# Performance work log

Measured on AMD Instinct MI355X. Metric: run time of the kernel, lower is better.

Reference implementation:

```python
import jax, jax.numpy as jnp
import numpy as np

D_MODEL = 2048
N_HEADS = 16
KV_HEADS = 4
HEAD_DIM = D_MODEL // N_HEADS  # 128
GROUP = N_HEADS // KV_HEADS    # 4
B, T = 2, 2048
KV_WIDTH = KV_HEADS * HEAD_DIM


def _alibi_bias(n_heads: int, t: int) -> jnp.ndarray:
    # standard alibi slopes: geometric sequence 2^(-8i/n)
    slopes = 2.0 ** (-8.0 * (np.arange(1, n_heads + 1) / n_heads))
    rel = np.arange(t)[None, :] - np.arange(t)[:, None]  # j - i (<=0 in causal region)
    bias = slopes[:, None, None] * rel[None, :, :]
    return jnp.asarray(bias[None], dtype=jnp.float32)  # [1, H, T, T]


def setup_inputs() -> dict:
    key = jax.random.key(0)
    ks = jax.random.split(key, 5)
    s = 0.02
    x = jax.random.normal(ks[0], (B, T, D_MODEL), dtype=jnp.float32)
    attn_mask = jnp.tril(jnp.ones((T, T), dtype=bool))[None, None]  # [1,1,T,T]
    alibi_bias = _alibi_bias(N_HEADS, T)
    qkv_w = jax.random.normal(ks[1], (D_MODEL + 2 * KV_WIDTH, D_MODEL), dtype=jnp.float32) * s
    qkv_b = jax.random.normal(ks[2], (D_MODEL + 2 * KV_WIDTH,), dtype=jnp.float32) * s
    proj_w = jax.random.normal(ks[3], (D_MODEL, D_MODEL), dtype=jnp.float32) * s
    proj_b = jax.random.normal(ks[4], (D_MODEL,), dtype=jnp.float32) * s
    return {"x": x, "attn_mask": attn_mask, "alibi_bias": alibi_bias,
            "qkv_w": qkv_w, "qkv_b": qkv_b, "proj_w": proj_w, "proj_b": proj_b}


def reference(x, attn_mask, alibi_bias, qkv_w, qkv_b, proj_w, proj_b):
    b, t, c = x.shape
    qkv = x @ qkv_w.T + qkv_b  # [b, t, d + 2*kv_width]
    q = qkv[..., :D_MODEL]
    k = qkv[..., D_MODEL:D_MODEL + KV_WIDTH]
    v = qkv[..., D_MODEL + KV_WIDTH:]
    # grouped layout: query heads [b, kv, group, t, hd]; kv heads [b, kv, t, hd]
    q = q.reshape(b, t, KV_HEADS, GROUP, HEAD_DIM).transpose(0, 2, 3, 1, 4)
    k = k.reshape(b, t, KV_HEADS, HEAD_DIM).transpose(0, 2, 1, 3)
    v = v.reshape(b, t, KV_HEADS, HEAD_DIM).transpose(0, 2, 1, 3)
    scale = 1.0 / jnp.sqrt(jnp.asarray(HEAD_DIM, x.dtype))
    att = jnp.einsum('bkgtd,bksd->bkgts', q, k) * scale  # [b, kv, group, t, t]
    att = att + alibi_bias.reshape(1, KV_HEADS, GROUP, t, t)
    att = jnp.where(attn_mask[:, :, None], att, jnp.asarray(-jnp.inf, att.dtype))
    att = jax.nn.softmax(att, axis=-1)
    out = jnp.einsum('bkgts,bksd->bkgtd', att, v)  # [b, kv, group, t, hd]
    out = out.transpose(0, 3, 1, 2, 4).reshape(b, t, c)
    return out @ proj_w.T + proj_b
```

## Files before the change

### kernel.cpp

```cpp
#include <hip/hip_runtime.h>
#include <hip/hip_bf16.h>
#include <math.h>

typedef unsigned short u16;
typedef unsigned int   u32;
typedef __attribute__((ext_vector_type(8))) short bf16x8;
typedef __attribute__((ext_vector_type(4))) float f32x4;
typedef __attribute__((ext_vector_type(4))) unsigned short u16x4;
typedef __attribute__((ext_vector_type(4))) unsigned int   u32x4;

#define T_SEQ 2048
#define BATCH 2
#define NHEAD 16
#define KVHEADS 4
#define HD 128
#define DM 2048
#define QKV_N 3072
#define MROWS 4096

__device__ __forceinline__ float bf2f(u16 u) {
    union { u32 i; float f; } v; v.i = ((u32)u) << 16; return v.f;
}
__device__ __forceinline__ u16 f2bf(float f) {
    u32 x = __float_as_uint(f);
    u32 r = (x + 0x7fffu + ((x >> 16) & 1u)) >> 16;
    return (u16)r;
}

__device__ __forceinline__ void gl16(const void* g, void* lds) {
    __builtin_amdgcn_global_load_lds(
        (const __attribute__((address_space(1))) void*)g,
        (__attribute__((address_space(3))) void*)lds, 16, 0, 0);
}

__device__ __forceinline__ int alibi_w1(int h) {
    return (int)(36.0f * exp2f(0.5f * (float)(h + 1)) * (1.0f / 64.0f)) + 2;
}

__global__ void reset_u32(u32* p, u32 v) { *p = v; }

__global__ void cvt_f32_bf16(const float* __restrict__ in, u16* __restrict__ out, int nq)
{
    int i = blockIdx.x * blockDim.x + threadIdx.x;
    const int stride = gridDim.x * blockDim.x;
    for (; i < nq; i += stride) {
        f32x4 v = ((const f32x4*)in)[i];
        u16x4 o = { f2bf(v[0]), f2bf(v[1]), f2bf(v[2]), f2bf(v[3]) };
        ((u16x4*)out)[i] = o;
    }
}

template <int EPI>
__global__ __launch_bounds__(256, 3)
void gemm_bt(const u16* __restrict__ A, const u16* __restrict__ Bw,
             const float* __restrict__ bias, u16* __restrict__ C,
             float* __restrict__ Cf, u16* __restrict__ Vt, int M, int N, int K)
{
    __shared__ __align__(16) u16 As[128 * 64];
    __shared__ __align__(16) u16 Bs[128 * 64];

    const int tid = threadIdx.x;
    const int l = tid & 63;
    const int w = tid >> 6;
    const int wr = w >> 1, wc = w & 1;
    const int bm = blockIdx.x, bn = blockIdx.y;

    const int lrow = l >> 3;
    const int lsl  = (l & 7) ^ lrow;
    const size_t aBase = (size_t)(bm * 128 + w * 8 + lrow) * K + lsl * 8;
    const size_t bBase = (size_t)(bn * 128 + w * 8 + lrow) * K + lsl * 8;

    const int sw = (l & 7) << 4;
    int offA[4], offB[4];
#pragma unroll
    for (int mf = 0; mf < 4; ++mf)
        offA[mf] = (wr * 64 + mf * 16 + (l & 15)) * 128 + (((l >> 4) * 16) ^ sw);
#pragma unroll
    for (int nf = 0; nf < 4; ++nf)
        offB[nf] = (wc * 64 + nf * 16 + (l & 15)) * 128 + (((l >> 4) * 16) ^ sw);

    f32x4 acc[4][4];
#pragma unroll
    for (int i = 0; i < 4; ++i)
#pragma unroll
        for (int j = 0; j < 4; ++j)
            acc[i][j] = (f32x4){0.f, 0.f, 0.f, 0.f};

    const int nK = K >> 6;
    for (int kt = 0; kt < nK; ++kt) {
        __syncthreads();
#pragma unroll
        for (int j = 0; j < 4; ++j) {
            gl16(A  + aBase + (size_t)j * 32 * K + kt * 64,
                 (char*)As + (w * 8 + j * 32) * 128);
            gl16(Bw + bBase + (size_t)j * 32 * K + kt * 64,
                 (char*)Bs + (w * 8 + j * 32) * 128);
        }
        __syncthreads();
#pragma unroll
        for (int kk = 0; kk < 2; ++kk) {
            bf16x8 af[4], bfr[4];
#pragma unroll
            for (int mf = 0; mf < 4; ++mf)
                af[mf] = *(const bf16x8*)((const char*)As + (offA[mf] ^ (kk << 6)));
#pragma unroll
            for (int nf = 0; nf < 4; ++nf)
                bfr[nf] = *(const bf16x8*)((const char*)Bs + (offB[nf] ^ (kk << 6)));
            __builtin_amdgcn_s_setprio(1);
#pragma unroll
            for (int mf = 0; mf < 4; ++mf)
#pragma unroll
                for (int nf = 0; nf < 4; ++nf)
                    acc[mf][nf] = __builtin_amdgcn_mfma_f32_16x16x32_bf16(
                        af[mf], bfr[nf], acc[mf][nf], 0, 0, 0);
            __builtin_amdgcn_s_setprio(0);
        }
    }

    const int row0 = bm * 128 + wr * 64 + ((l >> 4) << 2);
    const int col0 = bn * 128 + wc * 64 + (l & 15);
#pragma unroll
    for (int mf = 0; mf < 4; ++mf) {
#pragma unroll
        for (int nf = 0; nf < 4; ++nf) {
            const int row = row0 + mf * 16;
            const int col = col0 + nf * 16;
            const float bv = bias[col];
            float v0 = acc[mf][nf][0] + bv;
            float v1 = acc[mf][nf][1] + bv;
            float v2 = acc[mf][nf][2] + bv;
            float v3 = acc[mf][nf][3] + bv;
            if (EPI == 0) {
                if (col < 2560) {
                    C[(size_t)(row + 0) * QKV_N + col] = f2bf(v0);
                    C[(size_t)(row + 1) * QKV_N + col] = f2bf(v1);
                    C[(size_t)(row + 2) * QKV_N + col] = f2bf(v2);
                    C[(size_t)(row + 3) * QKV_N + col] = f2bf(v3);
                } else {
                    const int dd = col - 2560;
                    const int kv = dd >> 7;
                    const int d = dd & 127;
                    const int bidx = row >> 11;
                    const int tt = row & 2047;
                    u16x4 pv = {f2bf(v0), f2bf(v1), f2bf(v2), f2bf(v3)};
                    *(u16x4*)(Vt + ((size_t)((bidx * KVHEADS + kv) * HD + d)) * T_SEQ + tt) = pv;
                }
            } else {
                Cf[(size_t)(row + 0) * DM + col] = v0;
                Cf[(size_t)(row + 1) * DM + col] = v1;
                Cf[(size_t)(row + 2) * DM + col] = v2;
                Cf[(size_t)(row + 3) * DM + col] = v3;
            }
        }
    }
}

#define PWS_SEG 8448
__global__ __launch_bounds__(256, 2)
void attn_fwd(const u16* __restrict__ qkv, const u16* __restrict__ Vt,
              u16* __restrict__ AO, u32* __restrict__ ctr,
              float* __restrict__ PWS)
{
    __shared__ __align__(16) u16 Ks[2 * 64 * 128];
    __shared__ __align__(16) u16 Vs[2 * 64 * 128];
    __shared__ __align__(16) u16 Ps[4 * 16 * 64];
    __shared__ int sh_item;

    const int tid = threadIdx.x;
    const int l = tid & 63;
    const int w = tid >> 6;

    const int sw = (l & 7) << 4;
    int offK0[4];
#pragma unroll
    for (int nf = 0; nf < 4; ++nf)
        offK0[nf] = (nf * 16 + (l & 15)) * 256 + (((l >> 4) * 16) ^ sw);

    const int ldChunk = w * 1024;
    const int kslot = ((l & 15) ^ ((4 * (w & 1)) | (l >> 4))) * 8;
    const int vslot = ((l & 7) ^ (l >> 3)) * 8;

    const float LOG2E = 1.4426950408889634f;
    const float scale2 = 0.08838834764831845f * LOG2E;
    const bf16x8 ones = {(short)0x3F80, (short)0x3F80, (short)0x3F80, (short)0x3F80,
                         (short)0x3F80, (short)0x3F80, (short)0x3F80, (short)0x3F80};

    int item = blockIdx.x;

    for (;;) {
        __syncthreads();
        if (item < 0 && tid == 0) sh_item = (int)atomicAdd(ctr, 1u);
        __syncthreads();
        if (item < 0) item = sh_item;
        if (item >= 1536) break;

        int seg, qt, bh;
        if (item < 512)       { seg = 0; qt = 31 - (item >> 5);          bh = item & 31; }
        else if (item < 1024) { seg = 1; qt = 31 - ((item - 512) >> 5);  bh = item & 31; }
        else                  { seg = 0; qt = 15 - ((item - 1024) >> 5); bh = item & 31; }
        const int b = bh >> 4;
        const int h = bh & 15;
        const int kvh = h >> 2;
        const int q0 = qt << 6;

        const float slope2 = exp2f(-0.5f * (float)(h + 1)) * LOG2E;
        const int W1 = alibi_w1(h);
        const int jt_min = (qt - W1 > 0) ? (qt - W1) : 0;
        const bool split = (qt >= 16) && (W1 >= 16);
        if (seg == 1 && !split) { item = -1; continue; }

        const int jt_hi = seg ? (qt - 16) : qt;
        const int jt_lo = seg ? jt_min : (split ? (qt - 15) : jt_min);

        const size_t gK0 = (size_t)(b * T_SEQ + 4 * w + (l >> 4)) * QKV_N
                           + 2048 + kvh * HD + kslot;
        const size_t gV0 = (size_t)((b * KVHEADS + kvh) * HD + 8 * w + (l >> 3)) * T_SEQ
                           + vslot;

        const size_t qrow_off = (size_t)h * HD + ((l >> 4) << 3);
        bf16x8 qreg[4];
#pragma unroll
        for (int kk = 0; kk < 4; ++kk)
            qreg[kk] = *(const bf16x8*)(qkv +
                (size_t)(b * T_SEQ + q0 + w * 16 + (l & 15)) * QKV_N + qrow_off + kk * 32);

        float m_run[4];
        f32x4 o[8];
        f32x4 lacc = (f32x4){0.f, 0.f, 0.f, 0.f};
#pragma unroll
        for (int i = 0; i < 4; ++i) m_run[i] = -1e30f;
#pragma unroll
        for (int nf = 0; nf < 8; ++nf) o[nf] = (f32x4){0.f, 0.f, 0.f, 0.f};

        const int tb = q0 + w * 16 + ((l >> 4) << 2);
        const float dslope = slope2 * 64.0f;
        float abase[4][4];
#pragma unroll
        for (int nf = 0; nf < 4; ++nf)
#pragma unroll
            for (int i = 0; i < 4; ++i)
                abase[nf][i] = slope2 * (float)((jt_hi << 6) + nf * 16 + (l & 15) - (tb + i));

#pragma unroll
        for (int j = 0; j < 4; ++j) {
            gl16(qkv + gK0 + (size_t)((jt_hi << 6) + 16 * j) * QKV_N,
                 (char*)Ks + ldChunk + j * 4096);
            gl16(Vt + gV0 + (size_t)(32 * j) * T_SEQ + (jt_hi << 6),
                 (char*)Vs + ldChunk + j * 4096);
        }

        for (int c = 0, jt = jt_hi; jt >= jt_lo; --jt, ++c) {
            const int bsel = (c & 1) << 14;

            __syncthreads();

            if (jt > jt_lo) {
                const int ns0 = (jt - 1) << 6;
                const int b2 = ((c + 1) & 1) << 14;
#pragma unroll
                for (int j = 0; j < 4; ++j) {
                    gl16(qkv + gK0 + (size_t)(ns0 + 16 * j) * QKV_N,
                         (char*)Ks + b2 + ldChunk + j * 4096);
                    gl16(Vt + gV0 + (size_t)(32 * j) * T_SEQ + ns0,
                         (char*)Vs + b2 + ldChunk + j * 4096);
                }
            }

            f32x4 sc[4];
#pragma unroll
            for (int nf = 0; nf < 4; ++nf) sc[nf] = (f32x4){0.f, 0.f, 0.f, 0.f};
            __builtin_amdgcn_s_setprio(1);
#pragma unroll
            for (int kk = 0; kk < 4; ++kk) {
#pragma unroll
                for (int nf = 0; nf < 4; ++nf) {
                    bf16x8 kb = *(const bf16x8*)((const char*)Ks + bsel + (offK0[nf] ^ (kk << 6)));
                    sc[nf] = __builtin_amdgcn_mfma_f32_16x16x32_bf16(qreg[kk], kb, sc[nf], 0, 0, 0);
                }
            }
            __builtin_amdgcn_s_setprio(0);

            float vals[4][4];
#pragma unroll
            for (int nf = 0; nf < 4; ++nf)
#pragma unroll
                for (int i = 0; i < 4; ++i) {
                    vals[nf][i] = fmaf(sc[nf][i], scale2, abase[nf][i]);
                    abase[nf][i] -= dslope;
                }
            if (seg == 0 && c == 0) {
                const int s0 = jt << 6;
#pragma unroll
                for (int nf = 0; nf < 4; ++nf) {
                    const int scol = s0 + nf * 16 + (l & 15);
#pragma unroll
                    for (int i = 0; i < 4; ++i)
                        if (scol > tb + i) vals[nf][i] = -__builtin_inff();
                }
            }

            float lm[4];
#pragma unroll
            for (int i = 0; i < 4; ++i)
                lm[i] = fmaxf(fmaxf(vals[0][i], vals[1][i]), fmaxf(vals[2][i], vals[3][i]));
            const bool ok = (lm[0] <= m_run[0] + 10.f) && (lm[1] <= m_run[1] + 10.f) &&
                            (lm[2] <= m_run[2] + 10.f) && (lm[3] <= m_run[3] + 10.f);
            if (!__all(ok)) {
                float corr[4];
#pragma unroll
                for (int i = 0; i < 4; ++i) {
                    float mx = lm[i];
#pragma unroll
                    for (int d = 1; d < 16; d <<= 1) mx = fmaxf(mx, __shfl_xor(mx, d, 64));
                    const float mn = fmaxf(m_run[i], mx);
                    corr[i] = exp2f(m_run[i] - mn);
                    m_run[i] = mn;
                }
#pragma unroll
                for (int nf = 0; nf < 8; ++nf) {
                    o[nf][0] *= corr[0]; o[nf][1] *= corr[1];
                    o[nf][2] *= corr[2]; o[nf][3] *= corr[3];
                }
                lacc[0] *= corr[0]; lacc[1] *= corr[1];
                lacc[2] *= corr[2]; lacc[3] *= corr[3];
            }

            const int pbase = w * 2048;
#pragma unroll
            for (int nf = 0; nf < 4; ++nf)
#pragma unroll
                for (int i = 0; i < 4; ++i) {
                    const float p = exp2f(vals[nf][i] - m_run[i]);
                    const int r = ((l >> 4) << 2) + i;
                    const int off = pbase + ((r * 128 + nf * 32 + ((l & 15) << 1)) ^ ((r & 7) << 4));
                    *(u16*)((char*)Ps + off) = f2bf(p);
                }

            const int rp = l & 15;
            __builtin_amdgcn_s_setprio(1);
#pragma unroll
            for (int kk = 0; kk < 2; ++kk) {
                bf16x8 pfr = *(const bf16x8*)((const char*)Ps + pbase +
                              (rp * 128 + ((((l >> 4) * 16) ^ sw) ^ (kk << 6))));
                lacc = __builtin_amdgcn_mfma_f32_16x16x32_bf16(pfr, ones, lacc, 0, 0, 0);
#pragma unroll
                for (int nf = 0; nf < 8; ++nf) {
                    const int offv = (nf * 16 + (l & 15)) * 128 + ((((l >> 4) * 16) ^ sw) ^ (kk << 6));
                    bf16x8 vb = *(const bf16x8*)((const char*)Vs + bsel + offv);
                    o[nf] = __builtin_amdgcn_mfma_f32_16x16x32_bf16(pfr, vb, o[nf], 0, 0, 0);
                }
            }
            __builtin_amdgcn_s_setprio(0);
        }

        if (!split) {
            float rinv[4];
#pragma unroll
            for (int i = 0; i < 4; ++i) rinv[i] = 1.f / lacc[i];
            const size_t orow = (size_t)(b * T_SEQ + q0 + w * 16 + ((l >> 4) << 2));
#pragma unroll
            for (int nf = 0; nf < 8; ++nf) {
                const int col = h * HD + nf * 16 + (l & 15);
#pragma unroll
                for (int i = 0; i < 4; ++i)
                    AO[(orow + i) * DM + col] = f2bf(o[nf][i] * rinv[i]);
            }
        } else {
            const int rid = (bh << 5) | qt;
            float* base = PWS + (size_t)(rid * 2 + seg) * PWS_SEG;
            const int row0 = w * 16 + ((l >> 4) << 2);
#pragma unroll
            for (int nf = 0; nf < 8; ++nf) {
                const int col = nf * 16 + (l & 15);
#pragma unroll
                for (int i = 0; i < 4; ++i)
                    base[(row0 + i) * 128 + col] = o[nf][i];
            }
            if ((l & 15) == 0) {
#pragma unroll
                for (int i = 0; i < 4; ++i) {
                    base[8192 + row0 + i] = m_run[i];
                    base[8256 + row0 + i] = lacc[i];
                }
            }
        }

        item = -1;
    }
}

__global__ __launch_bounds__(256)
void attn_combine(const float* __restrict__ PWS, u16* __restrict__ AO)
{
    const int rid = blockIdx.x;
    const int qt = rid & 31;
    const int bh = rid >> 5;
    const int b = bh >> 4;
    const int h = bh & 15;
    if (!(qt >= 16 && alibi_w1(h) >= 16)) return;

    const float* p0 = PWS + (size_t)(rid * 2 + 0) * PWS_SEG;
    const float* p1 = PWS + (size_t)(rid * 2 + 1) * PWS_SEG;

    const int t = threadIdx.x;
    const int row = t >> 2;
    const int c0 = (t & 3) * 32;

    const float m0 = p0[8192 + row], m1 = p1[8192 + row];
    const float l0 = p0[8256 + row], l1 = p1[8256 + row];
    const float m = fmaxf(m0, m1);
    const float w0 = exp2f(m0 - m), w1 = exp2f(m1 - m);
    const float rinv = 1.f / (l0 * w0 + l1 * w1);

    const size_t ao = (size_t)(b * T_SEQ + (qt << 6) + row) * DM + h * HD + c0;
#pragma unroll
    for (int j = 0; j < 32; ++j) {
        const float v = (p0[row * 128 + c0 + j] * w0 + p1[row * 128 + c0 + j] * w1) * rinv;
        AO[ao + j] = f2bf(v);
    }
}

extern "C" void kernel_launch(void* const* d_in, const int* in_sizes, int n_in,
                              void* d_out, int out_size, void* d_ws, size_t ws_size,
                              hipStream_t stream)
{
    const float* x      = (const float*)d_in[0];
    const float* qkv_w  = (const float*)d_in[3];
    const float* qkv_b  = (const float*)d_in[4];
    const float* proj_w = (const float*)d_in[5];
    const float* proj_b = (const float*)d_in[6];
    float* out = (float*)d_out;

    u16* ws  = (u16*)d_ws;
    u16* xb  = ws;
    u16* AO  = ws;
    u16* qwb = ws + 8388608;
    u16* pwb = qwb + 6291456;
    u16* qkv = pwb + 4194304;
    u16* Vt  = qkv + 12582912;
    u32* ctr = (u32*)(ws + 33554432);
    float* PWS = (float*)((char*)d_ws + 67108880);

    reset_u32<<<1, 1, 0, stream>>>(ctr, 512u);
    cvt_f32_bf16<<<2048, 256, 0, stream>>>(x,      xb,  8388608 / 4);
    cvt_f32_bf16<<<2048, 256, 0, stream>>>(qkv_w,  qwb, 6291456 / 4);
    cvt_f32_bf16<<<1024, 256, 0, stream>>>(proj_w, pwb, 4194304 / 4);

    gemm_bt<0><<<dim3(32, 24), 256, 0, stream>>>(xb, qwb, qkv_b, qkv, nullptr, Vt,
                                                 MROWS, QKV_N, DM);
    attn_fwd<<<dim3(512), 256, 0, stream>>>(qkv, Vt, AO, ctr, PWS);
    attn_combine<<<dim3(1024), 256, 0, stream>>>(PWS, AO);
    gemm_bt<1><<<dim3(32, 16), 256, 0, stream>>>(AO, pwb, proj_b, nullptr, out, nullptr,
                                                 MROWS, DM, DM);
}
```

Before: 193.6 us.

## Single-buffer attention K/V tiles, double occupancy, and remap work items by XCD

The attention kernel drops double-buffered K/V shared memory and loads the next tile after the PV MMA behind an extra barrier. The freed LDS allows launch bounds of 4 blocks per CU and a 1024-block launch. The work-item decode now spreads heads across XCDs and enumerates only the split second-segment items, so no atomics are wasted on skipped items. The alibi base is kept as a per-row term plus per-fragment constants to save registers. In exchange, K/V load latency is no longer hidden behind compute within a block and must be covered by the extra resident blocks.

```diff
diff --git a/kernel.cpp b/kernel.cpp
--- a/kernel.cpp
+++ b/kernel.cpp
@@ -156,15 +156,14 @@
 }
 
 #define PWS_SEG 8448
-__global__ __launch_bounds__(256, 2)
+__global__ __launch_bounds__(256, 4)
 void attn_fwd(const u16* __restrict__ qkv, const u16* __restrict__ Vt,
               u16* __restrict__ AO, u32* __restrict__ ctr,
               float* __restrict__ PWS)
 {
-    __shared__ __align__(16) u16 Ks[2 * 64 * 128];
-    __shared__ __align__(16) u16 Vs[2 * 64 * 128];
+    __shared__ __align__(16) u16 Ks[64 * 128];
+    __shared__ __align__(16) u16 Vs[64 * 128];
     __shared__ __align__(16) u16 Ps[4 * 16 * 64];
-    __shared__ int sh_item;
 
     const int tid = threadIdx.x;
     const int l = tid & 63;
@@ -189,25 +188,36 @@
 
     for (;;) {
         __syncthreads();
-        if (item < 0 && tid == 0) sh_item = (int)atomicAdd(ctr, 1u);
+        if (item < 0 && tid == 0)
+            *(volatile int*)Ps = (int)atomicAdd(ctr, 1u);
         __syncthreads();
-        if (item < 0) item = sh_item;
-        if (item >= 1536) break;
-
-        int seg, qt, bh;
-        if (item < 512)       { seg = 0; qt = 31 - (item >> 5);          bh = item & 31; }
-        else if (item < 1024) { seg = 1; qt = 31 - ((item - 512) >> 5);  bh = item & 31; }
-        else                  { seg = 0; qt = 15 - ((item - 1024) >> 5); bh = item & 31; }
-        const int b = bh >> 4;
-        const int h = bh & 15;
+        if (item < 0) item = *(volatile int*)Ps;
+        if (item >= 1248) break;
+
+        int seg, qt, b, h;
+        if (item < 1024) {
+            const int xcd = item & 7, slot = item >> 3;
+            b = xcd >> 2;
+            h = (xcd & 3) * 4 + (slot & 3);
+            qt = 31 - (slot >> 2);
+            seg = 0;
+        } else {
+            const int idx = item - 1024;
+            const int qtd = idx / 14;
+            const int r = idx - qtd * 14;
+            qt = 31 - qtd;
+            h = 9 + (r % 7);
+            b = r / 7;
+            seg = 1;
+        }
         const int kvh = h >> 2;
+        const int bh = (b << 4) | h;
         const int q0 = qt << 6;
 
         const float slope2 = exp2f(-0.5f * (float)(h + 1)) * LOG2E;
         const int W1 = alibi_w1(h);
         const int jt_min = (qt - W1 > 0) ? (qt - W1) : 0;
-        const bool split = (qt >= 16) && (W1 >= 16);
-        if (seg == 1 && !split) { item = -1; continue; }
+        const bool split = (qt >= 16) && (h >= 9);
 
         const int jt_hi = seg ? (qt - 16) : qt;
         const int jt_lo = seg ? jt_min : (split ? (qt - 15) : jt_min);
@@ -234,12 +244,13 @@
 
         const int tb = q0 + w * 16 + ((l >> 4) << 2);
         const float dslope = slope2 * 64.0f;
-        float abase[4][4];
-#pragma unroll
-        for (int nf = 0; nf < 4; ++nf)
-#pragma unroll
-            for (int i = 0; i < 4; ++i)
-                abase[nf][i] = slope2 * (float)((jt_hi << 6) + nf * 16 + (l & 15) - (tb + i));
+        float basei[4];
+#pragma unroll
+        for (int i = 0; i < 4; ++i)
+            basei[i] = slope2 * (float)((jt_hi << 6) + (l & 15) - (tb + i));
+        float cnf[4];
+#pragma unroll
+        for (int nf = 0; nf < 4; ++nf) cnf[nf] = slope2 * (float)(nf * 16);
 
 #pragma unroll
         for (int j = 0; j < 4; ++j) {
@@ -250,21 +261,7 @@
         }
 
         for (int c = 0, jt = jt_hi; jt >= jt_lo; --jt, ++c) {
-            const int bsel = (c & 1) << 14;
-
             __syncthreads();
-
-            if (jt > jt_lo) {
-                const int ns0 = (jt - 1) << 6;
-                const int b2 = ((c + 1) & 1) << 14;
-#pragma unroll
-                for (int j = 0; j < 4; ++j) {
-                    gl16(qkv + gK0 + (size_t)(ns0 + 16 * j) * QKV_N,
-                         (char*)Ks + b2 + ldChunk + j * 4096);
-                    gl16(Vt + gV0 + (size_t)(32 * j) * T_SEQ + ns0,
-                         (char*)Vs + b2 + ldChunk + j * 4096);
-                }
-            }
 
             f32x4 sc[4];
 #pragma unroll
@@ -274,7 +271,7 @@
             for (int kk = 0; kk < 4; ++kk) {
 #pragma unroll
                 for (int nf = 0; nf < 4; ++nf) {
-                    bf16x8 kb = *(const bf16x8*)((const char*)Ks + bsel + (offK0[nf] ^ (kk << 6)));
+                    bf16x8 kb = *(const bf16x8*)((const char*)Ks + (offK0[nf] ^ (kk << 6)));
                     sc[nf] = __builtin_amdgcn_mfma_f32_16x16x32_bf16(qreg[kk], kb, sc[nf], 0, 0, 0);
                 }
             }
@@ -284,10 +281,11 @@
 #pragma unroll
             for (int nf = 0; nf < 4; ++nf)
 #pragma unroll
-                for (int i = 0; i < 4; ++i) {
-                    vals[nf][i] = fmaf(sc[nf][i], scale2, abase[nf][i]);
-                    abase[nf][i] -= dslope;
-                }
+                for (int i = 0; i < 4; ++i)
+                    vals[nf][i] = fmaf(sc[nf][i], scale2, basei[i] + cnf[nf]);
+#pragma unroll
+            for (int i = 0; i < 4; ++i) basei[i] -= dslope;
+
             if (seg == 0 && c == 0) {
                 const int s0 = jt << 6;
 #pragma unroll
@@ -346,11 +344,23 @@
 #pragma unroll
                 for (int nf = 0; nf < 8; ++nf) {
                     const int offv = (nf * 16 + (l & 15)) * 128 + ((((l >> 4) * 16) ^ sw) ^ (kk << 6));
-                    bf16x8 vb = *(const bf16x8*)((const char*)Vs + bsel + offv);
+                    bf16x8 vb = *(const bf16x8*)((const char*)Vs + offv);
                     o[nf] = __builtin_amdgcn_mfma_f32_16x16x32_bf16(pfr, vb, o[nf], 0, 0, 0);
                 }
             }
             __builtin_amdgcn_s_setprio(0);
+
+            if (jt > jt_lo) {
+                __syncthreads();
+                const int ns0 = (jt - 1) << 6;
+#pragma unroll
+                for (int j = 0; j < 4; ++j) {
+                    gl16(qkv + gK0 + (size_t)(ns0 + 16 * j) * QKV_N,
+                         (char*)Ks + ldChunk + j * 4096);
+                    gl16(Vt + gV0 + (size_t)(32 * j) * T_SEQ + ns0,
+                         (char*)Vs + ldChunk + j * 4096);
+                }
+            }
         }
 
         if (!split) {
@@ -441,14 +451,14 @@
     u32* ctr = (u32*)(ws + 33554432);
     float* PWS = (float*)((char*)d_ws + 67108880);
 
-    reset_u32<<<1, 1, 0, stream>>>(ctr, 512u);
+    reset_u32<<<1, 1, 0, stream>>>(ctr, 1024u);
     cvt_f32_bf16<<<2048, 256, 0, stream>>>(x,      xb,  8388608 / 4);
     cvt_f32_bf16<<<2048, 256, 0, stream>>>(qkv_w,  qwb, 6291456 / 4);
     cvt_f32_bf16<<<1024, 256, 0, stream>>>(proj_w, pwb, 4194304 / 4);
 
     gemm_bt<0><<<dim3(32, 24), 256, 0, stream>>>(xb, qwb, qkv_b, qkv, nullptr, Vt,
                                                  MROWS, QKV_N, DM);
-    attn_fwd<<<dim3(512), 256, 0, stream>>>(qkv, Vt, AO, ctr, PWS);
+    attn_fwd<<<dim3(1024), 256, 0, stream>>>(qkv, Vt, AO, ctr, PWS);
     attn_combine<<<dim3(1024), 256, 0, stream>>>(PWS, AO);
     gemm_bt<1><<<dim3(32, 16), 256, 0, stream>>>(AO, pwb, proj_b, nullptr, out, nullptr,
                                                  MROWS, DM, DM);
```

After: 236.4 us. 22.2% more time.
